# Kernel optimization log

Hardware: AMD Instinct MI355X
Metric: run time of the kernel (lower is better)

Reference implementation:

```python
import jax, jax.numpy as jnp
import numpy as np

N = 100000
E = 3200000

def gcn_conv(x, W, b, src, dst, num_nodes):
    # PyG GCNConv: x' = D^-1/2 (A+I) D^-1/2 (x W) + b
    h = x @ W  # [N, out]
    # self loops appended
    src_sl = jnp.concatenate([src, jnp.arange(num_nodes)])
    dst_sl = jnp.concatenate([dst, jnp.arange(num_nodes)])
    deg = jnp.zeros((num_nodes,), h.dtype).at[dst_sl].add(1.0)
    dinv = jnp.where(deg > 0, 1.0 / jnp.sqrt(deg), 0.0)
    norm = dinv[src_sl] * dinv[dst_sl]  # [E+N]
    msgs = h[src_sl] * norm[:, None]
    out = jnp.zeros_like(h).at[dst_sl].add(msgs)
    return out + b

def setup_inputs() -> dict:
    key = jax.random.key(0)
    k1, k2, k3, k4, k5 = jax.random.split(key, 5)
    z = jax.random.normal(k1, (N, 16), dtype=jnp.float32)
    edge_index = jax.random.randint(k2, (2, E), 0, N, dtype=jnp.int64)
    W1 = jax.random.normal(k3, (16, 256), dtype=jnp.float32) * (1.0 / np.sqrt(16))
    b1 = jnp.zeros((256,), jnp.float32)
    W2 = jax.random.normal(k4, (256, 256), dtype=jnp.float32) * (1.0 / np.sqrt(256))
    b2 = jnp.zeros((256,), jnp.float32)
    return {"z": z, "edge_index": edge_index, "W1": W1, "b1": b1, "W2": W2, "b2": b2}

def reference(z, edge_index, W1, b1, W2, b2):
    src, dst = edge_index[0], edge_index[1]
    h = gcn_conv(z, W1, b1, src, dst, N)
    h = gcn_conv(h, W2, b2, src, dst, N)
    value = jnp.sum(h[src] * h[dst], axis=1)  # [E]
    return jax.nn.sigmoid(value)
```

## Files before the change

### kernel.cpp

```cpp
#include <hip/hip_runtime.h>
#include <hip/hip_fp16.h>
#include <math.h>

#define N_NODES 100000
#define N_EDGES 3200000
#define GRID_N 391
#define GRID_G 6250
#define NSB 782
#define SB_NODES 128
#define SBCAP 5120
#define E_BLK 12800
#define PART_BLOCKS 250
#define PART_THREADS 1024
#define QUART_E 800000
#define GRID_D 3125

#define OFF_DINV 0
#define OFF_C    100016
#define OFF_ZS16 200032
#define OFF_T16  1000048
#define OFF_U    1800064
#define OFF_YT   3400080
#define OFF_PR   6604720
#define OFF_PB   6604736
#define OFF_ABG  6604752
#define OFF_L    6604768
#define FLOAT_TOTAL 6605024
#define IOFF_GCUR 0
#define IOFF_BEG  1024
#define IOFF_CNT  101024
#define IOFF_BUF  201024
#define IOFF_CSR  4204864

__device__ inline float4 h4_to_f4(uint2 v) {
    __half2 a = *reinterpret_cast<__half2*>(&v.x);
    __half2 b = *reinterpret_cast<__half2*>(&v.y);
    float2 fa = __half22float2(a), fb = __half22float2(b);
    return make_float4(fa.x, fa.y, fb.x, fb.y);
}
__device__ inline uint2 f4_to_h4(float4 f) {
    uint2 r;
    __half2 a = __floats2half2_rn(f.x, f.y);
    __half2 b = __floats2half2_rn(f.z, f.w);
    r.x = *reinterpret_cast<unsigned*>(&a);
    r.y = *reinterpret_cast<unsigned*>(&b);
    return r;
}
__device__ inline float4 pack_h8(float4 a, float4 b) {
    float4 r;
    __half2* p = reinterpret_cast<__half2*>(&r);
    p[0] = __floats2half2_rn(a.x, a.y);
    p[1] = __floats2half2_rn(a.z, a.w);
    p[2] = __floats2half2_rn(b.x, b.y);
    p[3] = __floats2half2_rn(b.z, b.w);
    return r;
}
__device__ inline unsigned h2bits(float a, float b) {
    __half2 h = __floats2half2_rn(a, b);
    return *reinterpret_cast<unsigned*>(&h);
}
__device__ inline float2 bits2f2(unsigned v) {
    __half2 h = *reinterpret_cast<__half2*>(&v);
    return __half22float2(h);
}
__device__ inline float hdot2w(unsigned wa, unsigned wb) {
    float2 fa = bits2f2(wa), fb = bits2f2(wb);
    return fa.x * fb.x + fa.y * fb.y;
}
__device__ inline void acc4(float4& acc, uint2 g) {
    float4 f = h4_to_f4(g);
    acc.x += f.x; acc.y += f.y; acc.z += f.z; acc.w += f.w;
}

struct ConstsSh {
    float sW1t[16 * 256];
    float sM[16 * 257];
    float sb1[256];
    float sb2[256];
    float sR[256];
    float sG[256];
    float sLf[256];
};
struct PartSh {
    int hist[4][NSB];
    int cur[NSB];
};

__global__ void __launch_bounds__(PART_THREADS)
k_part(const int* __restrict__ src, const int* __restrict__ dst,
       int* __restrict__ gcur, int* __restrict__ buf,
       const float* __restrict__ W1, const float* __restrict__ b1,
       const float* __restrict__ W2, const float* __restrict__ b2,
       float* __restrict__ ws) {
    __shared__ union { ConstsSh c; PartSh p; } sh;
    int t = threadIdx.x;

    if (blockIdx.x == PART_BLOCKS) {
        bool act = t < 256;
        if (act) {
            #pragma unroll
            for (int r = 0; r < 16; r++)
                sh.c.sW1t[t * 16 + r] = W1[r * 256 + t];
            sh.c.sb1[t] = b1[t];
            sh.c.sb2[t] = b2[t];
        }
        __syncthreads();
        if (act) {
            float acc[16];
            #pragma unroll
            for (int i = 0; i < 16; i++) acc[i] = 0.0f;
            float raccv = 0.0f;
            for (int kk = 0; kk < 256; kk += 8) {
                float w2v[8];
                #pragma unroll
                for (int u = 0; u < 8; u++)
                    w2v[u] = W2[(kk + u) * 256 + t];
                #pragma unroll
                for (int u = 0; u < 8; u++) {
                    #pragma unroll
                    for (int i = 0; i < 16; i++)
                        acc[i] += sh.c.sW1t[(kk + u) * 16 + i] * w2v[u];
                    raccv += sh.c.sb1[kk + u] * w2v[u];
                }
            }
            #pragma unroll
            for (int i = 0; i < 16; i++) sh.c.sM[i * 257 + t] = acc[i];
            sh.c.sR[t] = raccv;
        }
        __syncthreads();
        if (act) {
            int i = t >> 4, j = t & 15;
            float gg = 0.0f;
            for (int tt = 0; tt < 256; tt++)
                gg += sh.c.sM[i * 257 + tt] * sh.c.sM[j * 257 + tt];
            sh.c.sG[t] = gg;
        }
        if (t < 16) {
            float a = 0.0f, b = 0.0f;
            for (int tt = 0; tt < 256; tt++) {
                a += sh.c.sM[t * 257 + tt] * sh.c.sR[tt];
                b += sh.c.sM[t * 257 + tt] * sh.c.sb2[tt];
            }
            ws[OFF_PR + t] = a;
            ws[OFF_PB + t] = b;
        }
        if (t == 0) {
            float al = 0.0f, be = 0.0f, ga = 0.0f;
            for (int tt = 0; tt < 256; tt++) {
                al += sh.c.sR[tt] * sh.c.sR[tt];
                be += sh.c.sR[tt] * sh.c.sb2[tt];
                ga += sh.c.sb2[tt] * sh.c.sb2[tt];
            }
            float disc = sqrtf(al * al + 4.0f);
            float lp = 0.5f * (al + disc);
            float lm = 0.5f * (al - disc);
            float k1 = sqrtf(lp / (lp * lp + 1.0f));
            float k2 = sqrtf(-lm / (lm * lm + 1.0f));
            ws[OFF_ABG + 0] = be;
            ws[OFF_ABG + 1] = 0.5f * ga;
            ws[OFF_ABG + 2] = lp;
            ws[OFF_ABG + 3] = lm;
            ws[OFF_ABG + 4] = k1;
            ws[OFF_ABG + 5] = k2;
        }
        __syncthreads();
        if (act) sh.c.sLf[t] = 0.0f;
        __syncthreads();
        for (int j = 0; j < 16; j++) {
            if (t == j) {
                float s = sh.c.sG[j * 16 + j];
                for (int k = 0; k < j; k++)
                    s -= sh.c.sLf[j * 16 + k] * sh.c.sLf[j * 16 + k];
                sh.c.sLf[j * 16 + j] = sqrtf(fmaxf(s, 1e-20f));
            }
            __syncthreads();
            if (t > j && t < 16) {
                float s = sh.c.sG[t * 16 + j];
                for (int k = 0; k < j; k++)
                    s -= sh.c.sLf[t * 16 + k] * sh.c.sLf[j * 16 + k];
                sh.c.sLf[t * 16 + j] = s / sh.c.sLf[j * 16 + j];
            }
            __syncthreads();
        }
        if (act) ws[OFF_L + t] = sh.c.sLf[t];
        return;
    }

    int cp = t >> 8;
    int base = blockIdx.x * E_BLK;
    for (int i = t; i < 4 * NSB; i += PART_THREADS) ((int*)sh.p.hist)[i] = 0;
    __syncthreads();
    for (int i = t; i < E_BLK; i += PART_THREADS) {
        int e = base + i;
        if (e < N_EDGES)
            atomicAdd(&sh.p.hist[cp][__builtin_nontemporal_load(dst + e) >> 7], 1);
    }
    __syncthreads();
    for (int i = t; i < NSB; i += PART_THREADS) {
        int h = sh.p.hist[0][i] + sh.p.hist[1][i] + sh.p.hist[2][i] + sh.p.hist[3][i];
        sh.p.cur[i] = (h > 0) ? atomicAdd(&gcur[i], h) : 0;
    }
    __syncthreads();
    for (int i = t; i < E_BLK; i += PART_THREADS) {
        int e = base + i;
        if (e >= N_EDGES) continue;
        int d = __builtin_nontemporal_load(dst + e);
        int s = __builtin_nontemporal_load(src + e);
        int sb = d >> 7;
        int pos = atomicAdd(&sh.p.cur[sb], 1);
        if (pos < SBCAP) buf[sb * SBCAP + pos] = s | ((d & 127) << 17);
    }
}

__global__ void k_sort(const float* __restrict__ z, const int* __restrict__ gcur,
                       const int* __restrict__ buf, int* __restrict__ csr,
                       int* __restrict__ begA, int* __restrict__ cntA,
                       float* __restrict__ ws) {
    __shared__ int pay[SBCAP];
    __shared__ int h[SB_NODES + 1];
    __shared__ int lcur[SB_NODES];
    __shared__ float sdv[SB_NODES];
    int sb = blockIdx.x, t = threadIdx.x;
    int n = gcur[sb];
    if (n > SBCAP) n = SBCAP;
    for (int i = t; i < n; i += 256) pay[i] = buf[sb * SBCAP + i];
    if (t <= SB_NODES) h[t] = 0;
    __syncthreads();
    for (int i = t; i < n; i += 256) atomicAdd(&h[(pay[i] >> 17) + 1], 1);
    __syncthreads();
    int mydeg = 0;
    if (t < SB_NODES) { mydeg = h[t + 1]; h[t + 1] = (mydeg + 3) & ~3; }
    __syncthreads();
    for (int off = 1; off <= SB_NODES; off <<= 1) {
        int v = 0;
        if (t <= SB_NODES && t >= off) v = h[t - off];
        __syncthreads();
        if (t <= SB_NODES) h[t] += v;
        __syncthreads();
    }
    int n0 = sb * SB_NODES;
    if (t < SB_NODES) {
        lcur[t] = h[t];
        float dv = rsqrtf((float)(mydeg + 1));
        sdv[t] = dv;
        if (n0 + t < N_NODES) {
            cntA[n0 + t] = mydeg;
            begA[n0 + t] = sb * SBCAP + h[t];
            ws[OFF_DINV + n0 + t] = dv;
        }
    }
    __syncthreads();
    {
        int nl = t >> 1, half = t & 1;
        int node = n0 + nl;
        if (node < N_NODES) {
            const float4* zr = (const float4*)(z + (size_t)node * 16) + 2 * half;
            float dv = sdv[nl];
            float4 a = zr[0], b = zr[1];
            a = make_float4(a.x * dv, a.y * dv, a.z * dv, a.w * dv);
            b = make_float4(b.x * dv, b.y * dv, b.z * dv, b.w * dv);
            ((float4*)((__half*)(ws + OFF_ZS16) + (size_t)node * 16))[half] = pack_h8(a, b);
        }
    }
    for (int i = t; i < n; i += 256) {
        int p = pay[i];
        int dl = p >> 17;
        int pos = atomicAdd(&lcur[dl], 1);
        if (pos < SBCAP) csr[sb * SBCAP + pos] = p & 0x1FFFF;
    }
}

__global__ void k_gather1(const int* __restrict__ cntA, const int* __restrict__ begA,
                          const int* __restrict__ csr, float* __restrict__ ws) {
    int lane = threadIdx.x & 15;
    int g = threadIdx.x >> 4;
    int q = lane & 3;
    int sub = lane >> 2;
    int d = blockIdx.x * 16 + g;
    if (d >= N_NODES) return;
    const float* dinv = ws + OFF_DINV;
    const __half* zs = (const __half*)(ws + OFF_ZS16);
    float dd = dinv[d];
    float dv2 = dd * dd;
    int deg = cntA[d];
    int beg = begA[d];
    float4 acc = make_float4(0.f, 0.f, 0.f, 0.f);
    float csum = 0.0f;
    int j = 0;
    for (; j + 32 <= deg; j += 32) {
        int4 ia = *(const int4*)(csr + beg + j + sub * 4);
        int4 ib = *(const int4*)(csr + beg + j + 16 + sub * 4);
        uint2 g0 = ((const uint2*)(zs + (size_t)ia.x * 16))[q];
        uint2 g1 = ((const uint2*)(zs + (size_t)ia.y * 16))[q];
        uint2 g2 = ((const uint2*)(zs + (size_t)ia.z * 16))[q];
        uint2 g3 = ((const uint2*)(zs + (size_t)ia.w * 16))[q];
        uint2 g4 = ((const uint2*)(zs + (size_t)ib.x * 16))[q];
        uint2 g5 = ((const uint2*)(zs + (size_t)ib.y * 16))[q];
        uint2 g6 = ((const uint2*)(zs + (size_t)ib.z * 16))[q];
        uint2 g7 = ((const uint2*)(zs + (size_t)ib.w * 16))[q];
        acc4(acc, g0); acc4(acc, g1); acc4(acc, g2); acc4(acc, g3);
        acc4(acc, g4); acc4(acc, g5); acc4(acc, g6); acc4(acc, g7);
        if (q == 0)
            csum += ((dinv[ia.x] + dinv[ia.y]) + (dinv[ia.z] + dinv[ia.w]))
                  + ((dinv[ib.x] + dinv[ib.y]) + (dinv[ib.z] + dinv[ib.w]));
    }
    for (; j + 16 <= deg; j += 16) {
        int4 idx = *(const int4*)(csr + beg + j + sub * 4);
        uint2 g0 = ((const uint2*)(zs + (size_t)idx.x * 16))[q];
        uint2 g1 = ((const uint2*)(zs + (size_t)idx.y * 16))[q];
        uint2 g2 = ((const uint2*)(zs + (size_t)idx.z * 16))[q];
        uint2 g3 = ((const uint2*)(zs + (size_t)idx.w * 16))[q];
        acc4(acc, g0); acc4(acc, g1); acc4(acc, g2); acc4(acc, g3);
        if (q == 0) csum += (dinv[idx.x] + dinv[idx.y]) + (dinv[idx.z] + dinv[idx.w]);
    }
    for (int t = j + sub; t < deg; t += 4) {
        int s0 = csr[beg + t];
        acc4(acc, ((const uint2*)(zs + (size_t)s0 * 16))[q]);
        if (q == 0) csum += dinv[s0];
    }
    #pragma unroll
    for (int off = 4; off <= 8; off <<= 1) {
        acc.x += __shfl_xor(acc.x, off, 64);
        acc.y += __shfl_xor(acc.y, off, 64);
        acc.z += __shfl_xor(acc.z, off, 64);
        acc.w += __shfl_xor(acc.w, off, 64);
        csum  += __shfl_xor(csum,  off, 64);
    }
    if (sub == 0) {
        float4 zrow = h4_to_f4(((const uint2*)(zs + (size_t)d * 16))[q]);
        float4 o = make_float4(dv2 * (acc.x + zrow.x), dv2 * (acc.y + zrow.y),
                               dv2 * (acc.z + zrow.z), dv2 * (acc.w + zrow.w));
        ((uint2*)((__half*)(ws + OFF_T16) + (size_t)d * 16))[q] = f4_to_h4(o);
        if (q == 0) (ws + OFF_C)[d] = dd * csum + dv2;
    }
}

__global__ void k_gather2(const int* __restrict__ cntA, const int* __restrict__ begA,
                          const int* __restrict__ csr, float* __restrict__ ws) {
    int lane = threadIdx.x & 15;
    int g = threadIdx.x >> 4;
    int q = lane & 3;
    int sub = lane >> 2;
    int d = blockIdx.x * 16 + g;
    if (d >= N_NODES) return;
    const float* dinv = ws + OFF_DINV;
    const __half* t16 = (const __half*)(ws + OFF_T16);
    float dd = dinv[d];
    int deg = cntA[d];
    int beg = begA[d];
    float4 acc = make_float4(0.f, 0.f, 0.f, 0.f);
    int j = 0;
    for (; j + 32 <= deg; j += 32) {
        int4 ia = *(const int4*)(csr + beg + j + sub * 4);
        int4 ib = *(const int4*)(csr + beg + j + 16 + sub * 4);
        uint2 g0 = ((const uint2*)(t16 + (size_t)ia.x * 16))[q];
        uint2 g1 = ((const uint2*)(t16 + (size_t)ia.y * 16))[q];
        uint2 g2 = ((const uint2*)(t16 + (size_t)ia.z * 16))[q];
        uint2 g3 = ((const uint2*)(t16 + (size_t)ia.w * 16))[q];
        uint2 g4 = ((const uint2*)(t16 + (size_t)ib.x * 16))[q];
        uint2 g5 = ((const uint2*)(t16 + (size_t)ib.y * 16))[q];
        uint2 g6 = ((const uint2*)(t16 + (size_t)ib.z * 16))[q];
        uint2 g7 = ((const uint2*)(t16 + (size_t)ib.w * 16))[q];
        acc4(acc, g0); acc4(acc, g1); acc4(acc, g2); acc4(acc, g3);
        acc4(acc, g4); acc4(acc, g5); acc4(acc, g6); acc4(acc, g7);
    }
    for (; j + 16 <= deg; j += 16) {
        int4 idx = *(const int4*)(csr + beg + j + sub * 4);
        uint2 g0 = ((const uint2*)(t16 + (size_t)idx.x * 16))[q];
        uint2 g1 = ((const uint2*)(t16 + (size_t)idx.y * 16))[q];
        uint2 g2 = ((const uint2*)(t16 + (size_t)idx.z * 16))[q];
        uint2 g3 = ((const uint2*)(t16 + (size_t)idx.w * 16))[q];
        acc4(acc, g0); acc4(acc, g1); acc4(acc, g2); acc4(acc, g3);
    }
    for (int t = j + sub; t < deg; t += 4) {
        int s0 = csr[beg + t];
        acc4(acc, ((const uint2*)(t16 + (size_t)s0 * 16))[q]);
    }
    #pragma unroll
    for (int off = 4; off <= 8; off <<= 1) {
        acc.x += __shfl_xor(acc.x, off, 64);
        acc.y += __shfl_xor(acc.y, off, 64);
        acc.z += __shfl_xor(acc.z, off, 64);
        acc.w += __shfl_xor(acc.w, off, 64);
    }
    if (sub == 0) {
        float4 trow = h4_to_f4(((const uint2*)(t16 + (size_t)d * 16))[q]);
        float4 o = make_float4(dd * (acc.x + trow.x), dd * (acc.y + trow.y),
                               dd * (acc.z + trow.z), dd * (acc.w + trow.w));
        ((float4*)(ws + OFF_U + (size_t)d * 16))[q] = o;
    }
}

__global__ void k_pack(float* __restrict__ ws) {
    __shared__ float sL[256];
    __shared__ float spr[16];
    __shared__ float spb[16];
    __shared__ float sprm[8];
    int tid = threadIdx.x;
    sL[tid] = ws[OFF_L + tid];
    if (tid < 16) { spr[tid] = ws[OFF_PR + tid]; spb[tid] = ws[OFF_PB + tid]; }
    if (tid < 8) sprm[tid] = ws[OFF_ABG + tid];
    __syncthreads();
    int i = blockIdx.x * blockDim.x + tid;
    if (i >= N_NODES) return;
    const float* u = ws + OFF_U;
    const float* c = ws + OFF_C;
    float ur[16];
    const float4* urow = (const float4*)(u + (size_t)i * 16);
    #pragma unroll
    for (int m = 0; m < 4; m++) {
        float4 a = urow[m];
        ur[4 * m + 0] = a.x; ur[4 * m + 1] = a.y;
        ur[4 * m + 2] = a.z; ur[4 * m + 3] = a.w;
    }
    float A = 0.0f, B = 0.0f;
    #pragma unroll
    for (int kk = 0; kk < 16; kk++) { A += ur[kk] * spr[kk]; B += ur[kk] * spb[kk]; }
    float y[16];
    #pragma unroll
    for (int j = 0; j < 16; j++) {
        float accv = 0.0f;
        #pragma unroll
        for (int kk = 0; kk < 16; kk++) accv += ur[kk] * sL[kk * 16 + j];
        y[j] = accv;
    }
    float beta = sprm[0], gh = sprm[1], lp = sprm[2], lm = sprm[3];
    float k1 = sprm[4], k2 = sprm[5];
    float ci = c[i];
    float Ap = A + beta;
    float Bp = B + gh;
    float r1 = k1 * (lp * ci + Ap);
    float r2 = k2 * (lm * ci + Ap);
    const float inv_s2 = 0.70710678118654752f;
    float r3 = (Bp + 1.0f) * inv_s2;
    float r4 = (Bp - 1.0f) * inv_s2;
    uint2* rec = (uint2*)(ws + OFF_YT) + 5 * (size_t)i;
    rec[0] = make_uint2(h2bits(y[0],  y[1]),  h2bits(y[2],  y[3]));
    rec[1] = make_uint2(h2bits(y[4],  y[5]),  h2bits(y[6],  y[7]));
    rec[2] = make_uint2(h2bits(y[8],  y[9]),  h2bits(y[10], y[11]));
    rec[3] = make_uint2(h2bits(y[12], y[13]), h2bits(y[14], y[15]));
    rec[4] = make_uint2(h2bits(r1, r2), h2bits(r3, r4));
}

__global__ void __launch_bounds__(256, 4)
k_decode(const int* __restrict__ src, const int* __restrict__ dst,
         const float* __restrict__ ws, float* __restrict__ out) {
    int e0 = blockIdx.x * blockDim.x + threadIdx.x;
    if (e0 >= QUART_E) return;
    const uint2* yt = (const uint2*)(ws + OFF_YT);
    int s[4], d[4];
    #pragma unroll
    for (int k = 0; k < 4; k++) {
        int e = e0 + k * QUART_E;
        s[k] = __builtin_nontemporal_load(src + e);
        d[k] = __builtin_nontemporal_load(dst + e);
    }
    uint2 sr[4][5], dr[4][5];
    #pragma unroll
    for (int k = 0; k < 4; k++) {
        const uint2* rs = yt + 5 * (size_t)s[k];
        const uint2* rd = yt + 5 * (size_t)d[k];
        #pragma unroll
        for (int m = 0; m < 5; m++) { sr[k][m] = rs[m]; dr[k][m] = rd[m]; }
    }
    #pragma unroll
    for (int k = 0; k < 4; k++) {
        float v = 0.0f;
        #pragma unroll
        for (int m = 0; m < 4; m++) {
            v += hdot2w(sr[k][m].x, dr[k][m].x);
            v += hdot2w(sr[k][m].y, dr[k][m].y);
        }
        float2 ra = bits2f2(sr[k][4].x), rb = bits2f2(dr[k][4].x);
        float2 rc = bits2f2(sr[k][4].y), rd = bits2f2(dr[k][4].y);
        v += ra.x * rb.x - ra.y * rb.y + rc.x * rd.x - rc.y * rd.y;
        __builtin_nontemporal_store(1.0f / (1.0f + expf(-v)), out + e0 + k * QUART_E);
    }
}

extern "C" void kernel_launch(void* const* d_in, const int* in_sizes, int n_in,
                              void* d_out, int out_size, void* d_ws, size_t ws_size,
                              hipStream_t stream) {
    const float* z  = (const float*)d_in[0];
    const int*   ei = (const int*)d_in[1];
    const float* W1 = (const float*)d_in[2];
    const float* b1 = (const float*)d_in[3];
    const float* W2 = (const float*)d_in[4];
    const float* b2 = (const float*)d_in[5];
    float* out = (float*)d_out;
    float* ws  = (float*)d_ws;
    int*   wi  = (int*)(ws + FLOAT_TOTAL);

    const int* src = ei;
    const int* dst = ei + N_EDGES;

    int* gcur = wi + IOFF_GCUR;
    int* begA = wi + IOFF_BEG;
    int* cntA = wi + IOFF_CNT;
    int* buf  = wi + IOFF_BUF;
    int* csr  = wi + IOFF_CSR;

    hipMemsetAsync(gcur, 0, 1024 * sizeof(int), stream);
    k_part    <<<PART_BLOCKS + 1, PART_THREADS, 0, stream>>>(src, dst, gcur, buf,
                                                             W1, b1, W2, b2, ws);
    k_sort    <<<NSB, 256, 0, stream>>>(z, gcur, buf, csr, begA, cntA, ws);
    k_gather1 <<<GRID_G, 256, 0, stream>>>(cntA, begA, csr, ws);
    k_gather2 <<<GRID_G, 256, 0, stream>>>(cntA, begA, csr, ws);
    k_pack    <<<GRID_N, 256, 0, stream>>>(ws);
    k_decode  <<<GRID_D, 256, 0, stream>>>(src, dst, ws, out);
}
```

Baseline: 294.2 us.

## Split decode records into aligned 32-byte rows plus scalar side array

The per-node 40-byte fp16 record is split into a 32-byte-aligned block of 16 halves, read as two float4 loads, and a separate 8-byte side array for the scalar terms, placed at a new workspace offset. The decode gather then issues wider aligned loads instead of five uint2 loads per node. Sched barriers are also added in the aggregation loops so all gathers are issued before the accumulation math, and the dinv loads are moved ahead of the accumulations. Splitting the record adds a third gather stream per endpoint and depends on the new offset fitting inside the workspace regions already allocated.

```diff
diff --git a/kernel.cpp b/kernel.cpp
--- a/kernel.cpp
+++ b/kernel.cpp
@@ -21,6 +21,7 @@
 #define OFF_T16  1000048
 #define OFF_U    1800064
 #define OFF_YT   3400080
+#define OFF_ST   4200080
 #define OFF_PR   6604720
 #define OFF_PB   6604736
 #define OFF_ABG  6604752
@@ -63,9 +64,17 @@
     __half2 h = *reinterpret_cast<__half2*>(&v);
     return __half22float2(h);
 }
-__device__ inline float hdot2w(unsigned wa, unsigned wb) {
-    float2 fa = bits2f2(wa), fb = bits2f2(wb);
-    return fa.x * fb.x + fa.y * fb.y;
+__device__ inline float hdot8f(float4 a, float4 b) {
+    const __half2* pa = reinterpret_cast<const __half2*>(&a);
+    const __half2* pb = reinterpret_cast<const __half2*>(&b);
+    float s = 0.0f;
+    #pragma unroll
+    for (int i = 0; i < 4; i++) {
+        float2 fa = __half22float2(pa[i]);
+        float2 fb = __half22float2(pb[i]);
+        s += fa.x * fb.x + fa.y * fb.y;
+    }
+    return s;
 }
 __device__ inline void acc4(float4& acc, uint2 g) {
     float4 f = h4_to_f4(g);
@@ -298,11 +307,15 @@
         uint2 g5 = ((const uint2*)(zs + (size_t)ib.y * 16))[q];
         uint2 g6 = ((const uint2*)(zs + (size_t)ib.z * 16))[q];
         uint2 g7 = ((const uint2*)(zs + (size_t)ib.w * 16))[q];
+        float dva = 0.0f, dvb = 0.0f;
+        if (q == 0) {
+            dva = (dinv[ia.x] + dinv[ia.y]) + (dinv[ia.z] + dinv[ia.w]);
+            dvb = (dinv[ib.x] + dinv[ib.y]) + (dinv[ib.z] + dinv[ib.w]);
+        }
+        __builtin_amdgcn_sched_barrier(0);
         acc4(acc, g0); acc4(acc, g1); acc4(acc, g2); acc4(acc, g3);
         acc4(acc, g4); acc4(acc, g5); acc4(acc, g6); acc4(acc, g7);
-        if (q == 0)
-            csum += ((dinv[ia.x] + dinv[ia.y]) + (dinv[ia.z] + dinv[ia.w]))
-                  + ((dinv[ib.x] + dinv[ib.y]) + (dinv[ib.z] + dinv[ib.w]));
+        csum += dva + dvb;
     }
     for (; j + 16 <= deg; j += 16) {
         int4 idx = *(const int4*)(csr + beg + j + sub * 4);
@@ -361,6 +374,7 @@
         uint2 g5 = ((const uint2*)(t16 + (size_t)ib.y * 16))[q];
         uint2 g6 = ((const uint2*)(t16 + (size_t)ib.z * 16))[q];
         uint2 g7 = ((const uint2*)(t16 + (size_t)ib.w * 16))[q];
+        __builtin_amdgcn_sched_barrier(0);
         acc4(acc, g0); acc4(acc, g1); acc4(acc, g2); acc4(acc, g3);
         acc4(acc, g4); acc4(acc, g5); acc4(acc, g6); acc4(acc, g7);
     }
@@ -434,12 +448,12 @@
     const float inv_s2 = 0.70710678118654752f;
     float r3 = (Bp + 1.0f) * inv_s2;
     float r4 = (Bp - 1.0f) * inv_s2;
-    uint2* rec = (uint2*)(ws + OFF_YT) + 5 * (size_t)i;
-    rec[0] = make_uint2(h2bits(y[0],  y[1]),  h2bits(y[2],  y[3]));
-    rec[1] = make_uint2(h2bits(y[4],  y[5]),  h2bits(y[6],  y[7]));
-    rec[2] = make_uint2(h2bits(y[8],  y[9]),  h2bits(y[10], y[11]));
-    rec[3] = make_uint2(h2bits(y[12], y[13]), h2bits(y[14], y[15]));
-    rec[4] = make_uint2(h2bits(r1, r2), h2bits(r3, r4));
+    float4* yt = (float4*)(ws + OFF_YT);
+    yt[2 * i]     = pack_h8(make_float4(y[0], y[1], y[2], y[3]),
+                            make_float4(y[4], y[5], y[6], y[7]));
+    yt[2 * i + 1] = pack_h8(make_float4(y[8], y[9], y[10], y[11]),
+                            make_float4(y[12], y[13], y[14], y[15]));
+    ((uint2*)(ws + OFF_ST))[i] = make_uint2(h2bits(r1, r2), h2bits(r3, r4));
 }
 
 __global__ void __launch_bounds__(256, 4)
@@ -447,7 +461,8 @@
          const float* __restrict__ ws, float* __restrict__ out) {
     int e0 = blockIdx.x * blockDim.x + threadIdx.x;
     if (e0 >= QUART_E) return;
-    const uint2* yt = (const uint2*)(ws + OFF_YT);
+    const float4* yt = (const float4*)(ws + OFF_YT);
+    const uint2*  st = (const uint2*)(ws + OFF_ST);
     int s[4], d[4];
     #pragma unroll
     for (int k = 0; k < 4; k++) {
@@ -455,24 +470,25 @@
         s[k] = __builtin_nontemporal_load(src + e);
         d[k] = __builtin_nontemporal_load(dst + e);
     }
-    uint2 sr[4][5], dr[4][5];
+    float4 sy0[4], sy1[4], dy0[4], dy1[4];
+    uint2 ssc[4], dsc[4];
     #pragma unroll
     for (int k = 0; k < 4; k++) {
-        const uint2* rs = yt + 5 * (size_t)s[k];
-        const uint2* rd = yt + 5 * (size_t)d[k];
-        #pragma unroll
-        for (int m = 0; m < 5; m++) { sr[k][m] = rs[m]; dr[k][m] = rd[m]; }
-    }
+        const float4* rs = yt + 2 * (size_t)s[k];
+        const float4* rd = yt + 2 * (size_t)d[k];
+        sy0[k] = rs[0];
+        sy1[k] = rs[1];
+        dy0[k] = rd[0];
+        dy1[k] = rd[1];
+        ssc[k] = st[s[k]];
+        dsc[k] = st[d[k]];
+    }
+    __builtin_amdgcn_sched_barrier(0);
     #pragma unroll
     for (int k = 0; k < 4; k++) {
-        float v = 0.0f;
-        #pragma unroll
-        for (int m = 0; m < 4; m++) {
-            v += hdot2w(sr[k][m].x, dr[k][m].x);
-            v += hdot2w(sr[k][m].y, dr[k][m].y);
-        }
-        float2 ra = bits2f2(sr[k][4].x), rb = bits2f2(dr[k][4].x);
-        float2 rc = bits2f2(sr[k][4].y), rd = bits2f2(dr[k][4].y);
+        float v = hdot8f(sy0[k], dy0[k]) + hdot8f(sy1[k], dy1[k]);
+        float2 ra = bits2f2(ssc[k].x), rb = bits2f2(dsc[k].x);
+        float2 rc = bits2f2(ssc[k].y), rd = bits2f2(dsc[k].y);
         v += ra.x * rb.x - ra.y * rb.y + rc.x * rd.x - rc.y * rd.y;
         __builtin_nontemporal_store(1.0f / (1.0f + expf(-v)), out + e0 + k * QUART_E);
     }
```

After: 290.4 us. About the same (-1.3%).
